# Optimization experiments

Hardware: AMD Instinct MI355X
Metric: run time of the kernel (lower is better)

The kernel has to match this reference:

```python
import jax, jax.numpy as jnp
from jax import lax
import numpy as np

N_QUBITS = 8


def _apply_1q(state, w, n, m00, m01, m10, m11):
    # state: (B, 2, 2, ..., 2); wire w lives on axis 1+w (wire 0 = most significant)
    st = jnp.moveaxis(state, 1 + w, -1)
    a0, a1 = st[..., 0], st[..., 1]
    b0 = m00 * a0 + m01 * a1
    b1 = m10 * a0 + m11 * a1
    st = jnp.stack([b0, b1], axis=-1)
    return jnp.moveaxis(st, -1, 1 + w)


def _apply_rx(state, theta, w, n):
    # RX(t) = [[cos t/2, -i sin t/2], [-i sin t/2, cos t/2]], per-batch theta
    shp = (-1,) + (1,) * (n - 1)
    c = jnp.cos(theta / 2).reshape(shp).astype(jnp.complex64)
    s = (-1j) * jnp.sin(theta / 2).reshape(shp).astype(jnp.complex64)
    return _apply_1q(state, w, n, c, s, s, c)


def _apply_rz(state, theta, w, n):
    # RZ(t) = diag(e^{-it/2}, e^{+it/2})
    shp = (-1,) + (1,) * (n - 1)
    e = jnp.exp(-0.5j * theta.astype(jnp.complex64)).reshape(shp)
    return _apply_1q(state, w, n, e, jnp.zeros_like(e), jnp.zeros_like(e), jnp.conj(e))


def _apply_cnot(state, ctrl, tgt, n):
    st = jnp.moveaxis(state, (1 + ctrl, 1 + tgt), (-2, -1))
    st = jnp.stack([st[..., 0, :], st[..., 1, ::-1]], axis=-2)
    return jnp.moveaxis(st, (-2, -1), (1 + ctrl, 1 + tgt))


def _circuit_probs(params):
    # params: (B, n). Simulate the fixed PennyLane circuit: for each wire w:
    # RX(params[w]) on w, RZ(params[(w+1)%n]) on w, CNOT(w, (w+1)%n).
    B, n = params.shape
    state = jnp.zeros((B, 2 ** n), jnp.complex64).at[:, 0].set(1.0)
    state = state.reshape((B,) + (2,) * n)
    for w in range(n):
        state = _apply_rx(state, params[:, w], w, n)
        state = _apply_rz(state, params[:, (w + 1) % n], w, n)
        state = _apply_cnot(state, w, (w + 1) % n, n)
    probs = jnp.abs(state.reshape(B, -1)) ** 2  # (B, 2^n), wire 0 most significant
    p = probs[:, :n]
    return p / jnp.sum(p, axis=1, keepdims=True)


def _qgate(W, b, x):
    params = x @ W.T + b  # (B, n_qubits)
    return _circuit_probs(params)


def setup_inputs() -> dict:
    key = jax.random.key(0)
    ks = jax.random.split(key, 9)
    S, B, D, N = 1024, 128, 256, N_QUBITS
    fan_in = D + N
    lim = 1.0 / np.sqrt(fan_in)
    u = lambda k, shape: jax.random.uniform(k, shape, jnp.float32, -lim, lim)
    return {
        "inputs": jax.random.normal(ks[0], (S, B, D), jnp.float32),
        "Wf": u(ks[1], (N, fan_in)), "bf": u(ks[2], (N,)),
        "Wi": u(ks[3], (N, fan_in)), "bi": u(ks[4], (N,)),
        "Wu": u(ks[5], (N, fan_in)), "bu": u(ks[6], (N,)),
        "Wo": u(ks[7], (N, fan_in)), "bo": u(ks[8], (N,)),
    }


def reference(inputs, Wf, bf, Wi, bi, Wu, bu, Wo, bo):
    S, B, D = inputs.shape
    N = Wf.shape[0]  # hidden_dim == n_qubits
    h0 = jnp.zeros((B, N), inputs.dtype)
    c0 = jnp.zeros((B, N), inputs.dtype)

    def step(carry, x):
        h, c = carry
        comb = jnp.concatenate([x, h], axis=1)  # (B, D+N)
        f = _qgate(Wf, bf, comb)
        i = _qgate(Wi, bi, comb)
        g = jnp.tanh(_qgate(Wu, bu, comb))
        o = _qgate(Wo, bo, comb)
        c_new = f * c + i * g
        h_new = o * jnp.tanh(c_new)
        return (h_new, c_new), h_new

    (h_n, c_n), outputs = lax.scan(step, (h0, c0), inputs)
    return outputs, h_n, c_n
```

## Files before the change

kernel.cpp:

```cpp
#include <hip/hip_runtime.h>

#define S_STEPS 1024
#define BATCH 128
#define NQ 8
#define XW_FLOATS (BATCH * 32 * 1024)

using v2f     = float __attribute__((ext_vector_type(2)));
using frag_ab = __attribute__((ext_vector_type(8))) short;
using frag_cd = __attribute__((ext_vector_type(4))) float;

#define INV2PI 0.15915494309189535f

template<int CTRL>
__device__ __forceinline__ float dppf(float x) {
  return __int_as_float(__builtin_amdgcn_update_dpp(0, __float_as_int(x), CTRL, 0xf, 0xf, true));
}
__device__ __forceinline__ float bperm(int addr, float v) {
  return __int_as_float(__builtin_amdgcn_ds_bpermute(addr, __float_as_int(v)));
}
__device__ __forceinline__ short f2bf(float f) {
  unsigned u = __float_as_uint(f);
  return (short)((u + 0x7FFFu + ((u >> 16) & 1u)) >> 16);
}
__device__ __forceinline__ float bf2f(short h) {
  return __uint_as_float(((unsigned)(unsigned short)h) << 16);
}

__global__ __launch_bounds__(256) void qlstm_pre(
    const float* __restrict__ x,
    const float* __restrict__ Wf, const float* __restrict__ bf_,
    const float* __restrict__ Wi, const float* __restrict__ bi,
    const float* __restrict__ Wu, const float* __restrict__ bu,
    const float* __restrict__ Wo, const float* __restrict__ bo,
    float* __restrict__ xw)
{
  const int lane = threadIdx.x & 63;
  const int gid  = blockIdx.x * 4 + (threadIdx.x >> 6);
  const int t0 = (gid >> 3) * 8;
  const int b0 = (gid & 7) * 16;
  const int m  = lane & 15;
  const int kg = lane >> 4;

  float bb[2];
  const float* wcol[2];
#pragma unroll
  for (int n = 0; n < 2; ++n) {
    int c = n * 16 + m;
    int g = c >> 3, w = c & 7;
    const float* bg = (g == 0) ? bf_ : (g == 1) ? bi : (g == 2) ? bu : bo;
    const float* Wg = (g == 0) ? Wf  : (g == 1) ? Wi : (g == 2) ? Wu : Wo;
    bb[n]   = bg[w] * INV2PI;
    wcol[n] = Wg + w * 264 + kg * 8;
  }

  frag_cd acc[8][2];
#pragma unroll
  for (int t = 0; t < 8; ++t)
#pragma unroll
    for (int n = 0; n < 2; ++n)
      acc[t][n] = (frag_cd){bb[n], bb[n], bb[n], bb[n]};

  const float* xbase = x + ((size_t)t0 * 128 + b0 + m) * 256 + kg * 8;

#pragma unroll 1
  for (int kk = 0; kk < 8; ++kk) {
    frag_ab bhi[2], blo[2];
#pragma unroll
    for (int n = 0; n < 2; ++n)
#pragma unroll
      for (int j = 0; j < 8; ++j) {
        float w = wcol[n][kk * 32 + j] * INV2PI;
        short h = f2bf(w);
        bhi[n][j] = h;
        blo[n][j] = f2bf(w - bf2f(h));
      }
#pragma unroll
    for (int t = 0; t < 8; ++t) {
      const float* xp = xbase + (size_t)t * 32768 + kk * 32;
      float4 xv0 = *(const float4*)(xp);
      float4 xv1 = *(const float4*)(xp + 4);
      float xf[8] = {xv0.x, xv0.y, xv0.z, xv0.w, xv1.x, xv1.y, xv1.z, xv1.w};
      frag_ab ahi, alo;
#pragma unroll
      for (int j = 0; j < 8; ++j) {
        short h = f2bf(xf[j]);
        ahi[j] = h;
        alo[j] = f2bf(xf[j] - bf2f(h));
      }
#pragma unroll
      for (int n = 0; n < 2; ++n) {
        acc[t][n] = __builtin_amdgcn_mfma_f32_16x16x32_bf16(ahi, bhi[n], acc[t][n], 0, 0, 0);
        acc[t][n] = __builtin_amdgcn_mfma_f32_16x16x32_bf16(alo, bhi[n], acc[t][n], 0, 0, 0);
        acc[t][n] = __builtin_amdgcn_mfma_f32_16x16x32_bf16(ahi, blo[n], acc[t][n], 0, 0, 0);
      }
    }
  }

#pragma unroll
  for (int n = 0; n < 2; ++n)
#pragma unroll
    for (int rho = 0; rho < 4; ++rho) {
      float* op = xw + ((size_t)((b0 + kg * 4 + rho) * 32 + n * 16 + m)) * 1024 + t0;
      float4 v0 = {acc[0][n][rho], acc[1][n][rho], acc[2][n][rho], acc[3][n][rho]};
      float4 v1 = {acc[4][n][rho], acc[5][n][rho], acc[6][n][rho], acc[7][n][rho]};
      *(float4*)op = v0;
      *(float4*)(op + 4) = v1;
    }
}

__global__ __launch_bounds__(64) void qlstm_seq(
    const float* __restrict__ xw,
    const float* __restrict__ Wf, const float* __restrict__ Wi,
    const float* __restrict__ Wu, const float* __restrict__ Wo,
    float* __restrict__ out)
{
  const int lane = threadIdx.x;
  const int r = lane & 15, g = r >> 2, k = r & 3;
  const int b = blockIdx.x * 4 + (lane >> 4);
  const int B6 = (k >> 1) & 1, B7 = k & 1;
  const bool isB7 = (B7 != 0);
  const float s6 = B6 ? -1.f : 1.f,        o6 = B6 ? 1.f : 0.f;
  const float s7 = (B7^B6) ? -1.f : 1.f,   o7 = (B7^B6) ? 1.f : 0.f;
  const int wA = (k == 0) ? 0 : (k == 1) ? 5 : 7;
  const int wB = (k == 0) ? 1 : (k == 1) ? 6 : 7;

  const float* Wg = (g == 0) ? Wf : (g == 1) ? Wi : (g == 2) ? Wu : Wo;
  v2f whA2[4], whB2[4];
#pragma unroll
  for (int j2 = 0; j2 < 4; ++j2) {
    whA2[j2] = (v2f){Wg[wA*264+256+2*j2] * INV2PI, Wg[wA*264+256+2*j2+1] * INV2PI};
    whB2[j2] = (v2f){Wg[wB*264+256+2*j2] * INV2PI, Wg[wB*264+256+2*j2+1] * INV2PI};
  }

  const int aF = (((lane & 48) | k) << 2);
  const int aI = aF + 16, aU = aF + 32, aO = aF + 48;

  v2f h2[4];
#pragma unroll
  for (int j = 0; j < 4; ++j) h2[j] = (v2f){0.f, 0.f};
  float cA = 0.f, cB = 0.f, hqA = 0.f, hqB = 0.f;

  const float* bxw = xw + (size_t)b * 32768;
  const float4* pA = (const float4*)(bxw + (size_t)(g * 8 + wA) * 1024);
  const float4* pB = (const float4*)(bxw + (size_t)(g * 8 + wB) * 1024);
  float4 curA = pA[0], nxtA = pA[1];
  float4 curB = pB[0], nxtB = pB[1];

  const int soff = b * 8 + r;
  float houtS[16];

#pragma unroll 1
  for (int Tb = 0; Tb < S_STEPS; Tb += 16) {
#pragma unroll
    for (int sg = 0; sg < 4; ++sg) {
      int gi = (Tb >> 2) + sg;
      int tp = gi + 2; tp = (tp > 255) ? 255 : tp;
      float4 nnA = pA[tp], nnB = pB[tp];
#pragma unroll
      for (int u = 0; u < 4; ++u) {
        float xa = (u==0)?curA.x:(u==1)?curA.y:(u==2)?curA.z:curA.w;
        float xb = (u==0)?curB.x:(u==1)?curB.y:(u==2)?curB.z:curB.w;
        v2f accA = whA2[0]*h2[0]; accA = whA2[1]*h2[1] + accA;
        accA = whA2[2]*h2[2] + accA; accA = whA2[3]*h2[3] + accA;
        v2f accB = whB2[0]*h2[0]; accB = whB2[1]*h2[1] + accB;
        accB = whB2[2]*h2[2] + accB; accB = whB2[3]*h2[3] + accB;
        float pa = (xa + accA.x) + accA.y;
        float pb = (xb + accB.x) + accB.y;
        float ccA = fmaf(0.5f, __builtin_amdgcn_cosf(pa), 0.5f);
        float ccB = fmaf(0.5f, __builtin_amdgcn_cosf(pb), 0.5f);

        float C0 = dppf<0x00>(ccA), C1 = dppf<0x00>(ccB);
        float C5 = dppf<0x55>(ccA), C6 = dppf<0x55>(ccB);
        float C7 = dppf<0xAA>(ccA);

        float S0v = 1.f - C0, S1v = 1.f - C1;
        float P01 = C0 * C1, Q01 = S0v * S1v;
        float sel01 = isB7 ? Q01 : P01;
        float F7  = fmaf(s7, C7, o7);
        float F6A = fmaf(s6, C6, o6);
        float e7  = sel01 * F7;
        float dA  = C5 * F6A;
        float dB  = (1.f + dA) - (C5 + F6A);
        float d56 = C5 * C6;
        float U0  = fmaf(2.f, d56, 1.f - (C5 + C6));
        float S7v = 1.f - C7;
        float T0  = fmaf(fmaf(2.f, C7, -1.f), U0, S7v);
        float sden = fmaf(P01 - Q01, T0, Q01);
        float es  = e7 * __builtin_amdgcn_rcpf(sden);
        float pnA = es * dA, pnB = es * dB;

        float fvA = bperm(aF, pnA), ivA = bperm(aI, pnA);
        float uvA = bperm(aU, pnA), ovA = bperm(aO, pnA);
        float fvB = bperm(aF, pnB), ivB = bperm(aI, pnB);
        float uvB = bperm(aU, pnB), ovB = bperm(aO, pnB);

        float t2A = uvA * uvA;
        float gvA = uvA * (t2A + 15.f) * __builtin_amdgcn_rcpf(fmaf(6.f, t2A, 15.f));
        cA = fmaf(fvA, cA, ivA * gvA);
        float eA = __builtin_amdgcn_exp2f(fminf(cA, 15.f) * 2.88539008f);
        hqA = ovA * fmaf(-2.f, __builtin_amdgcn_rcpf(eA + 1.f), 1.f);
        float t2B = uvB * uvB;
        float gvB = uvB * (t2B + 15.f) * __builtin_amdgcn_rcpf(fmaf(6.f, t2B, 15.f));
        cB = fmaf(fvB, cB, ivB * gvB);
        float eB = __builtin_amdgcn_exp2f(fminf(cB, 15.f) * 2.88539008f);
        hqB = ovB * fmaf(-2.f, __builtin_amdgcn_rcpf(eB + 1.f), 1.f);

        h2[0].x = dppf<0x00>(hqA); h2[0].y = dppf<0x55>(hqA);
        h2[1].x = dppf<0xAA>(hqA); h2[1].y = dppf<0xFF>(hqA);
        h2[2].x = dppf<0x00>(hqB); h2[2].y = dppf<0x55>(hqB);
        h2[3].x = dppf<0xAA>(hqB); h2[3].y = dppf<0xFF>(hqB);

        houtS[sg * 4 + u] = (g == 0) ? hqA : hqB;
      }
      curA = nxtA; nxtA = nnA;
      curB = nxtB; nxtB = nnB;
    }
    if (r < 8) {
      float* op = out + (size_t)Tb * (BATCH * NQ) + soff;
#pragma unroll
      for (int tt = 0; tt < 16; ++tt)
        op[(size_t)tt * (BATCH * NQ)] = houtS[tt];
    }
  }
  if (r < 8) {
    size_t o1 = (size_t)S_STEPS * BATCH * NQ + soff;
    out[o1] = (g == 0) ? hqA : hqB;
    out[o1 + (size_t)BATCH * NQ] = (g == 0) ? cA : cB;
  }
}

extern "C" void kernel_launch(void* const* d_in, const int* in_sizes, int n_in,
                              void* d_out, int out_size, void* d_ws, size_t ws_size,
                              hipStream_t stream) {
  const float* x  = (const float*)d_in[0];
  const float* Wf = (const float*)d_in[1];
  const float* bf = (const float*)d_in[2];
  const float* Wi = (const float*)d_in[3];
  const float* bi = (const float*)d_in[4];
  const float* Wu = (const float*)d_in[5];
  const float* bu = (const float*)d_in[6];
  const float* Wo = (const float*)d_in[7];
  const float* bo = (const float*)d_in[8];
  float* xw  = (float*)d_ws;
  float* out = (float*)d_out;

  qlstm_pre<<<256, 256, 0, stream>>>(x, Wf, bf, Wi, bi, Wu, bu, Wo, bo, xw);
  qlstm_seq<<<32, 64, 0, stream>>>(xw, Wf, Wi, Wu, Wo, out);
}
```

Baseline: 459.0 us.

## Stage split-bf16 weights in LDS and retile input projection per batch row

The precompute kernel now converts all 32 weight columns once per block into hi/lo bf16 halves held in shared memory, instead of every wave re-reading and re-converting them from global memory. The work is retiled so each wave handles one batch element over 16 timesteps, with weights as the A operand and x as the B operand. The x loads are software-prefetched one K-chunk ahead, and the grid grows to 1024 blocks of 512 threads for more parallelism. In exchange, x is now read with a strided per-timestep pattern, output stores become scalar rather than float4, and each block redoes the weight conversion.

```diff
diff --git a/kernel.cpp b/kernel.cpp
--- a/kernel.cpp
+++ b/kernel.cpp
@@ -26,7 +26,7 @@
   return __uint_as_float(((unsigned)(unsigned short)h) << 16);
 }
 
-__global__ __launch_bounds__(256) void qlstm_pre(
+__global__ __launch_bounds__(512) void qlstm_pre(
     const float* __restrict__ x,
     const float* __restrict__ Wf, const float* __restrict__ bf_,
     const float* __restrict__ Wi, const float* __restrict__ bi,
@@ -34,78 +34,103 @@
     const float* __restrict__ Wo, const float* __restrict__ bo,
     float* __restrict__ xw)
 {
-  const int lane = threadIdx.x & 63;
-  const int gid  = blockIdx.x * 4 + (threadIdx.x >> 6);
-  const int t0 = (gid >> 3) * 8;
-  const int b0 = (gid & 7) * 16;
+  __shared__ short whi[32 * 264];
+  __shared__ short wlo[32 * 264];
+
+  const int tid = threadIdx.x;
+
+  {
+    const int base = tid * 16;
+    const int c = base >> 8, k0 = base & 255;
+    const int g = c >> 3, w = c & 7;
+    const float* Wg = (g == 0) ? Wf : (g == 1) ? Wi : (g == 2) ? Wu : Wo;
+    const float* p = Wg + w * 264 + k0;
+    const int o = c * 264 + k0;
+#pragma unroll
+    for (int q = 0; q < 2; ++q) {
+      float4 va = *(const float4*)(p + q * 8);
+      float4 vb = *(const float4*)(p + q * 8 + 4);
+      float vv[8] = {va.x, va.y, va.z, va.w, vb.x, vb.y, vb.z, vb.w};
+      frag_ab h8, l8;
+#pragma unroll
+      for (int j = 0; j < 8; ++j) {
+        float wv = vv[j] * INV2PI;
+        short h = f2bf(wv);
+        h8[j] = h;
+        l8[j] = f2bf(wv - bf2f(h));
+      }
+      *(frag_ab*)&whi[o + q * 8] = h8;
+      *(frag_ab*)&wlo[o + q * 8] = l8;
+    }
+  }
+  __syncthreads();
+
+  const int lane = tid & 63;
   const int m  = lane & 15;
   const int kg = lane >> 4;
-
-  float bb[2];
-  const float* wcol[2];
-#pragma unroll
-  for (int n = 0; n < 2; ++n) {
-    int c = n * 16 + m;
-    int g = c >> 3, w = c & 7;
-    const float* bg = (g == 0) ? bf_ : (g == 1) ? bi : (g == 2) ? bu : bo;
-    const float* Wg = (g == 0) ? Wf  : (g == 1) ? Wi : (g == 2) ? Wu : Wo;
-    bb[n]   = bg[w] * INV2PI;
-    wcol[n] = Wg + w * 264 + kg * 8;
-  }
-
-  frag_cd acc[8][2];
-#pragma unroll
-  for (int t = 0; t < 8; ++t)
-#pragma unroll
-    for (int n = 0; n < 2; ++n)
-      acc[t][n] = (frag_cd){bb[n], bb[n], bb[n], bb[n]};
-
-  const float* xbase = x + ((size_t)t0 * 128 + b0 + m) * 256 + kg * 8;
+  const int gid = blockIdx.x * 8 + (tid >> 6);
+  const int b  = gid >> 6;
+  const int t0 = (gid & 63) << 4;
+
+  float bb[2][4];
+#pragma unroll
+  for (int n = 0; n < 2; ++n)
+#pragma unroll
+    for (int r = 0; r < 4; ++r) {
+      int c = n * 16 + kg * 4 + r;
+      int g = c >> 3, w = c & 7;
+      const float* bg = (g == 0) ? bf_ : (g == 1) ? bi : (g == 2) ? bu : bo;
+      bb[n][r] = bg[w] * INV2PI;
+    }
+
+  const float* xbase = x + ((size_t)(t0 + m) * 128 + b) * 256 + kg * 8;
+  const int w0 = m * 264 + kg * 8;
+  const int w1 = w0 + 16 * 264;
+
+  frag_cd acc0 = {0.f, 0.f, 0.f, 0.f};
+  frag_cd acc1 = {0.f, 0.f, 0.f, 0.f};
+
+  float4 xv0 = *(const float4*)(xbase);
+  float4 xv1 = *(const float4*)(xbase + 4);
 
 #pragma unroll 1
   for (int kk = 0; kk < 8; ++kk) {
-    frag_ab bhi[2], blo[2];
-#pragma unroll
-    for (int n = 0; n < 2; ++n)
-#pragma unroll
-      for (int j = 0; j < 8; ++j) {
-        float w = wcol[n][kk * 32 + j] * INV2PI;
-        short h = f2bf(w);
-        bhi[n][j] = h;
-        blo[n][j] = f2bf(w - bf2f(h));
-      }
-#pragma unroll
-    for (int t = 0; t < 8; ++t) {
-      const float* xp = xbase + (size_t)t * 32768 + kk * 32;
-      float4 xv0 = *(const float4*)(xp);
-      float4 xv1 = *(const float4*)(xp + 4);
-      float xf[8] = {xv0.x, xv0.y, xv0.z, xv0.w, xv1.x, xv1.y, xv1.z, xv1.w};
-      frag_ab ahi, alo;
-#pragma unroll
-      for (int j = 0; j < 8; ++j) {
-        short h = f2bf(xf[j]);
-        ahi[j] = h;
-        alo[j] = f2bf(xf[j] - bf2f(h));
-      }
-#pragma unroll
-      for (int n = 0; n < 2; ++n) {
-        acc[t][n] = __builtin_amdgcn_mfma_f32_16x16x32_bf16(ahi, bhi[n], acc[t][n], 0, 0, 0);
-        acc[t][n] = __builtin_amdgcn_mfma_f32_16x16x32_bf16(alo, bhi[n], acc[t][n], 0, 0, 0);
-        acc[t][n] = __builtin_amdgcn_mfma_f32_16x16x32_bf16(ahi, blo[n], acc[t][n], 0, 0, 0);
-      }
-    }
-  }
-
-#pragma unroll
-  for (int n = 0; n < 2; ++n)
-#pragma unroll
-    for (int rho = 0; rho < 4; ++rho) {
-      float* op = xw + ((size_t)((b0 + kg * 4 + rho) * 32 + n * 16 + m)) * 1024 + t0;
-      float4 v0 = {acc[0][n][rho], acc[1][n][rho], acc[2][n][rho], acc[3][n][rho]};
-      float4 v1 = {acc[4][n][rho], acc[5][n][rho], acc[6][n][rho], acc[7][n][rho]};
-      *(float4*)op = v0;
-      *(float4*)(op + 4) = v1;
-    }
+    float4 nx0 = xv0, nx1 = xv1;
+    if (kk < 7) {
+      nx0 = *(const float4*)(xbase + (kk + 1) * 32);
+      nx1 = *(const float4*)(xbase + (kk + 1) * 32 + 4);
+    }
+    frag_ab a0h = *(const frag_ab*)&whi[w0 + kk * 32];
+    frag_ab a0l = *(const frag_ab*)&wlo[w0 + kk * 32];
+    frag_ab a1h = *(const frag_ab*)&whi[w1 + kk * 32];
+    frag_ab a1l = *(const frag_ab*)&wlo[w1 + kk * 32];
+
+    float xf[8] = {xv0.x, xv0.y, xv0.z, xv0.w, xv1.x, xv1.y, xv1.z, xv1.w};
+    frag_ab xh, xl;
+#pragma unroll
+    for (int j = 0; j < 8; ++j) {
+      short h = f2bf(xf[j]);
+      xh[j] = h;
+      xl[j] = f2bf(xf[j] - bf2f(h));
+    }
+
+    acc0 = __builtin_amdgcn_mfma_f32_16x16x32_bf16(a0h, xh, acc0, 0, 0, 0);
+    acc0 = __builtin_amdgcn_mfma_f32_16x16x32_bf16(a0l, xh, acc0, 0, 0, 0);
+    acc0 = __builtin_amdgcn_mfma_f32_16x16x32_bf16(a0h, xl, acc0, 0, 0, 0);
+    acc1 = __builtin_amdgcn_mfma_f32_16x16x32_bf16(a1h, xh, acc1, 0, 0, 0);
+    acc1 = __builtin_amdgcn_mfma_f32_16x16x32_bf16(a1l, xh, acc1, 0, 0, 0);
+    acc1 = __builtin_amdgcn_mfma_f32_16x16x32_bf16(a1h, xl, acc1, 0, 0, 0);
+
+    xv0 = nx0; xv1 = nx1;
+  }
+
+#pragma unroll
+  for (int n = 0; n < 2; ++n) {
+    const frag_cd a = n ? acc1 : acc0;
+#pragma unroll
+    for (int r = 0; r < 4; ++r)
+      xw[((size_t)(b * 32 + n * 16 + kg * 4 + r)) * 1024 + t0 + m] = a[r] + bb[n][r];
+  }
 }
 
 __global__ __launch_bounds__(64) void qlstm_seq(
@@ -244,6 +269,6 @@
   float* xw  = (float*)d_ws;
   float* out = (float*)d_out;
 
-  qlstm_pre<<<256, 256, 0, stream>>>(x, Wf, bf, Wi, bi, Wu, bu, Wo, bo, xw);
+  qlstm_pre<<<1024, 512, 0, stream>>>(x, Wf, bf, Wi, bi, Wu, bu, Wo, bo, xw);
   qlstm_seq<<<32, 64, 0, stream>>>(xw, Wf, Wi, Wu, Wo, out);
 }
```

After: 447.4 us. -2.5%, faster.
